# Kernel optimization log

Measured on AMD Instinct MI355X. Metric: run time of the kernel, lower is better.

## Reference

```python
import jax, jax.numpy as jnp
import numpy as np

T, B = 1024, 128
IDIM, CDIM, N, M = 256, 512, 128, 64


def setup_inputs() -> dict:
    key = jax.random.key(0)
    ks = jax.random.split(key, 10)
    stdev = 5.0 / np.sqrt(IDIM + M + CDIM)  # matches _reset_controller
    u = lambda k, shp: jax.random.uniform(k, shp, jnp.float32, -stdev, stdev)
    return {
        "embs": jax.random.normal(ks[0], (T, B, IDIM), jnp.float32),
        "ilen": T // 2,
        # LSTM controller params (PyTorch layout: [4*cdim, in] / [4*cdim, cdim])
        "w_ih": u(ks[1], (4 * CDIM, IDIM + M)),
        "w_hh": u(ks[2], (4 * CDIM, CDIM)),
        "b_ih": jnp.zeros((4 * CDIM,), jnp.float32),
        "b_hh": jnp.zeros((4 * CDIM,), jnp.float32),
        "h0": jax.random.normal(ks[3], (CDIM,), jnp.float32) * 0.05,
        "c0": jax.random.normal(ks[4], (CDIM,), jnp.float32) * 0.05,
        "r0": jax.random.normal(ks[5], (1, M), jnp.float32) * 0.02,
        # memory head params (concrete subclass): write address / write value / read address
        "W_wa": jax.random.normal(ks[6], (N, CDIM), jnp.float32) * 0.02,
        "b_wa": jnp.zeros((N,), jnp.float32),
        "W_wv": jax.random.normal(ks[7], (M, IDIM), jnp.float32) * 0.02,
        "b_wv": jnp.zeros((M,), jnp.float32),
        "W_ra": jax.random.normal(ks[8], (N, CDIM), jnp.float32) * 0.02,
        "b_ra": jnp.zeros((N,), jnp.float32),
    }


def _forward(embs, w_ih, w_hh, b_ih, b_hh, h0, c0, r0,
             W_wa, b_wa, W_wv, b_wv, W_ra, b_ra, ilen):
    bsz = embs.shape[1]
    h = jnp.broadcast_to(h0, (bsz, CDIM))
    c = jnp.broadcast_to(c0, (bsz, CDIM))
    r = jnp.broadcast_to(r0, (bsz, M))
    mem = jnp.zeros((bsz, N, M), embs.dtype)
    b = b_ih + b_hh

    def step(carry, xt):
        h, c, r, mem = carry
        emb, t = xt  # emb: [B, idim]
        x = jnp.concatenate([emb, r], axis=-1)            # [B, idim+M]
        gates = x @ w_ih.T + h @ w_hh.T + b               # [B, 4*cdim]
        i, f, g, o = jnp.split(gates, 4, axis=-1)         # torch gate order i,f,g,o
        c_new = jax.nn.sigmoid(f) * c + jax.nn.sigmoid(i) * jnp.tanh(g)
        h_new = jax.nn.sigmoid(o) * jnp.tanh(c_new)       # controller_outp
        is_write = t < ilen
        # write(controller_outp, emb): additive write at softmax address
        wa = jax.nn.softmax(h_new @ W_wa.T + b_wa, axis=-1)   # [B, N]
        v = emb @ W_wv.T + b_wv                               # [B, M]
        mem_new = jnp.where(is_write, mem + wa[:, :, None] * v[:, None, :], mem)
        # read(controller_outp): softmax-addressed weighted sum over slots
        ra = jax.nn.softmax(h_new @ W_ra.T + b_ra, axis=-1)   # [B, N]
        r_read = jnp.einsum('bn,bnm->bm', ra, mem_new)        # [B, M]
        r_new = jnp.where(is_write, r, r_read)
        out = jnp.concatenate([h_new, r_new], axis=-1)        # [B, cdim+M]
        return (h_new, c_new, r_new, mem_new), out

    _, os = jax.lax.scan(step, (h, c, r, mem),
                         (embs, jnp.arange(embs.shape[0])))
    return os  # [T, B, cdim+M]


def reference(embs, ilen, w_ih, w_hh, b_ih, b_hh, h0, c0, r0,
              W_wa, b_wa, W_wv, b_wv, W_ra, b_ra):
    return _forward(embs, w_ih, w_hh, b_ih, b_hh, h0, c0, r0,
                    W_wa, b_wa, W_wv, b_wv, W_ra, b_ra, ilen)
```

## Files before the change

### kernel.cpp

```cpp
#include <hip/hip_runtime.h>

typedef _Float16 f16;
typedef __attribute__((ext_vector_type(8))) _Float16 half8;
typedef __attribute__((ext_vector_type(2))) _Float16 half2v;
typedef __attribute__((ext_vector_type(4))) float f32x4;
typedef __attribute__((ext_vector_type(4))) unsigned int u32x4;
typedef unsigned long long u64;

#define TSTEPS 1024

static const size_t OFF_WP   = 0;
static const size_t OFF_BIAS = 3407872;
static const size_t OFF_EMBP = 3416064;
static const size_t OFF_V    = 70524928;
static const size_t OFF_XPRH = 104079360;
static const size_t OFF_MEM  = 104374272;
static const size_t OFF_BAR  = 108568576;
static const size_t OFF_WVP  = 108569600;
static const size_t WS_NEED  = 108602368;


__global__ void marnn_packw(const float* __restrict__ w_ih, const float* __restrict__ w_hh,
                            const float* __restrict__ b_ih, const float* __restrict__ b_hh,
                            f16* __restrict__ WP, float* __restrict__ biasP) {
  int idx = blockIdx.x * 256 + threadIdx.x;
  if (idx < 2048) {
    int j = idx >> 2, g = idx & 3, rg = g * 512 + j;
    biasP[idx] = b_ih[rg] + b_hh[rg];
  }
  if (idx >= 1703936) return;
  int e = idx & 7, l = (idx >> 3) & 63;
  int q = idx >> 9;
  int ks = q % 26; int ntile = q / 26;
  int n = ntile * 16 + (l & 15);
  int k = ks * 32 + (l >> 4) * 8 + e;
  int j2 = n >> 2, g2 = n & 3, rg2 = g2 * 512 + j2;
  float v = (k < 320) ? w_ih[(size_t)rg2 * 320 + k] : w_hh[(size_t)rg2 * 512 + (k - 320)];
  WP[idx] = (f16)v;
}

__global__ void marnn_packwv(const float* __restrict__ W_wv, f16* __restrict__ WVP) {
  int idx = blockIdx.x * 256 + threadIdx.x;
  if (idx >= 16384) return;
  int e = idx & 7, l = (idx >> 3) & 63, ks = (idx >> 9) & 7, nt = idx >> 12;
  int n = nt * 16 + (l & 15);
  int k = ks * 32 + (l >> 4) * 8 + e;
  WVP[idx] = (f16)W_wv[n * 256 + k];
}

__global__ void marnn_packemb(const float* __restrict__ embs, f16* __restrict__ embsP) {
  const long total8 = (long)1024 * 128 * 32;
  const long stride = (long)gridDim.x * blockDim.x;
  for (long i8 = (long)blockIdx.x * blockDim.x + threadIdx.x; i8 < total8; i8 += stride) {
    int bl = (int)(i8 & 15), kc = (int)((i8 >> 4) & 31), bg = (int)((i8 >> 9) & 7);
    long t = i8 >> 12;
    const float* s = embs + ((t * 128) + bg * 16 + bl) * 256 + kc * 8;
    f32x4 a = *(const f32x4*)s, b = *(const f32x4*)(s + 4);
    half8 h;
    h[0]=(f16)a[0]; h[1]=(f16)a[1]; h[2]=(f16)a[2]; h[3]=(f16)a[3];
    h[4]=(f16)b[0]; h[5]=(f16)b[1]; h[6]=(f16)b[2]; h[7]=(f16)b[3];
    *(half8*)(embsP + i8 * 8) = h;
  }
}

__global__ __launch_bounds__(256)
void marnn_vpre(const f16* __restrict__ embsP, const f16* __restrict__ WVP,
                const float* __restrict__ b_wv, float* __restrict__ V) {
  const int tb = blockIdx.x;
  const int wv = threadIdx.x >> 6, l = threadIdx.x & 63;
  half8 bf[8];
  #pragma unroll
  for (int ks = 0; ks < 8; ++ks)
    bf[ks] = *(const half8*)(WVP + ((size_t)(wv * 8 + ks) * 64 + l) * 8);
  const f16* ab = embsP + (size_t)tb * 4096;
  f32x4 acc = {0.f, 0.f, 0.f, 0.f};
  #pragma unroll
  for (int ks = 0; ks < 8; ++ks) {
    half8 af = *(const half8*)(ab + ((size_t)(ks * 4 + (l >> 4)) * 16 + (l & 15)) * 8);
    acc = __builtin_amdgcn_mfma_f32_16x16x32_f16(bf[ks], af, acc, 0, 0, 0);
  }
  const int b = (tb & 7) * 16 + (l & 15);
  const long t = tb >> 3;
  #pragma unroll
  for (int r = 0; r < 4; ++r) {
    int m = wv * 16 + (l >> 4) * 4 + r;
    V[((t * 128) + b) * 64 + m] = acc[r] + b_wv[m];
  }
}

__global__ void marnn_init(const float* __restrict__ h0, const float* __restrict__ r0,
                           f16* __restrict__ XPRH) {
  int idx = blockIdx.x * 256 + threadIdx.x;
  if (idx >= 147456) return;
  int e = idx & 7; int q = idx >> 7; int kcidx = q % 72;
  float v = (kcidx < 8) ? r0[kcidx * 8 + e] : h0[(kcidx - 8) * 8 + e];
  XPRH[idx] = (f16)v;
}


struct __align__(16) MarnnSMem {
  f16  whead[128 * 512];
  char xl[26624];
  char un[4096];
};

__device__ __forceinline__ float marnn_dot8(half8 a, half8 b, float acc) {
#if __has_builtin(__builtin_amdgcn_fdot2)
  half2v a0 = {a[0],a[1]}, a1 = {a[2],a[3]}, a2 = {a[4],a[5]}, a3 = {a[6],a[7]};
  half2v b0 = {b[0],b[1]}, b1 = {b[2],b[3]}, b2 = {b[4],b[5]}, b3 = {b[6],b[7]};
  acc = __builtin_amdgcn_fdot2(a0, b0, acc, false);
  acc = __builtin_amdgcn_fdot2(a1, b1, acc, false);
  acc = __builtin_amdgcn_fdot2(a2, b2, acc, false);
  acc = __builtin_amdgcn_fdot2(a3, b3, acc, false);
#else
  #pragma unroll
  for (int e = 0; e < 8; ++e) acc += (float)a[e] * (float)b[e];
#endif
  return acc;
}

__device__ __forceinline__ float fast_sigmoid(float x) {
  return __builtin_amdgcn_rcpf(1.f + __expf(-x));
}
__device__ __forceinline__ float fast_tanh(float x) {
  return 1.f - 2.f * __builtin_amdgcn_rcpf(1.f + __expf(2.f * x));
}

__device__ __forceinline__ unsigned ld_flag(const unsigned* p) {
  return __hip_atomic_load(p, __ATOMIC_RELAXED, __HIP_MEMORY_SCOPE_AGENT);
}
__device__ __forceinline__ void st_flag(unsigned* p, unsigned v) {
  __hip_atomic_store(p, v, __ATOMIC_RELAXED, __HIP_MEMORY_SCOPE_AGENT);
}
__device__ __forceinline__ u64 ld_llc64(const void* p) {
  return __hip_atomic_load((const u64*)p, __ATOMIC_RELAXED, __HIP_MEMORY_SCOPE_AGENT);
}
__device__ __forceinline__ void st_llc32(void* p, unsigned v) {
  __hip_atomic_store((unsigned*)p, v, __ATOMIC_RELAXED, __HIP_MEMORY_SCOPE_AGENT);
}

__device__ __forceinline__ void poll16(const unsigned* line, unsigned ep) {
  int l = threadIdx.x & 63;
  for (;;) {
    unsigned v = (l < 16) ? ld_flag(line + l) : ep;
    if (__all((int)(v >= ep))) break;
    __builtin_amdgcn_s_sleep(1);
  }
  asm volatile("" ::: "memory");
}

union H2U { f16 f; unsigned short u; };

__global__ __launch_bounds__(512, 1)
void marnn_main(const int* __restrict__ ilen_p, const float* __restrict__ c0,
                const float* __restrict__ r0,
                const float* __restrict__ W_wa, const float* __restrict__ b_wa,
                const float* __restrict__ W_ra, const float* __restrict__ b_ra,
                float* __restrict__ out, char* __restrict__ ws) {
  __shared__ MarnnSMem sm;

  const f16*   WP    = (const f16*)(ws + OFF_WP);
  const float* biasP = (const float*)(ws + OFF_BIAS);
  const f16*   embsP = (const f16*)(ws + OFF_EMBP);
  const float* Vbuf  = (const float*)(ws + OFF_V);
  f16*         XPRH  = (f16*)(ws + OFF_XPRH);
  float*       MEMB  = (float*)(ws + OFF_MEM);
  unsigned*    FLAGS = (unsigned*)(ws + OFF_BAR);

  const int blk = blockIdx.x, tid = threadIdx.x;
  const int wav = tid >> 6, lane = tid & 63;
  const int g = blk & 7, ns = blk >> 3;
  const int ilen = ilen_p[0];
  unsigned* gfh = FLAGS + g * 32;
  unsigned* gfr = gfh + 16;

  half8 bfr[26];
  {
    const f16* wpb = WP + ((size_t)(ns * 8 + wav) * 26) * 512 + lane * 8;
    #pragma unroll
    for (int ks = 0; ks < 26; ++ks) bfr[ks] = *(const half8*)(wpb + ks * 512);
  }

  auto loadWhead = [&](const float* Wsrc) {
    for (int i = tid; i < 8192; i += 512) {
      int n = i >> 6, slot = i & 63;
      const float* s = Wsrc + n * 512 + slot * 8;
      f32x4 a = *(const f32x4*)(s), b2 = *(const f32x4*)(s + 4);
      half8 hv;
      hv[0]=(f16)a[0]; hv[1]=(f16)a[1]; hv[2]=(f16)a[2]; hv[3]=(f16)a[3];
      hv[4]=(f16)b2[0]; hv[5]=(f16)b2[1]; hv[6]=(f16)b2[2]; hv[7]=(f16)b2[3];
      *(half8*)((char*)sm.whead + (n << 10) + (((slot + n) & 63) << 4)) = hv;
    }
  };
  loadWhead(ilen > 0 ? W_wa : W_ra);

  {
    const u32x4* s0 = (const u32x4*)(embsP + ((size_t)0 * 8 + g) * 4096);
    ((u32x4*)sm.xl)[tid] = s0[tid];
    const u32x4* s1 = (const u32x4*)(XPRH + (((size_t)0 * 8 + g) * 72 + 8) * 128);
    u32x4* d1 = (u32x4*)(sm.xl + 10240);
    d1[tid * 2] = s1[tid * 2]; d1[tid * 2 + 1] = s1[tid * 2 + 1];
  }
  __syncthreads();

  const int b_l = tid >> 5, jj = tid & 31;
  const int jg = ns * 32 + jj;
  float c = c0[jg];
  const f32x4 bias4 = *(const f32x4*)(biasP + ns * 128 + jj * 4);
  const float r0v = (tid < 64) ? r0[tid] : 0.f;
  const int b = g * 16 + ns;

  const float bw0 = b_wa[lane], bw1 = b_wa[lane + 64];
  const float br0 = b_ra[lane], br1 = b_ra[lane + 64];
  const int gn = (wav & 3) * 32 + (lane & 31);
  const int kq = ((wav >> 2) << 1) | (lane >> 5);

  half8 rf0, rf1;
  {
    const f16* rbase = XPRH + ((size_t)g * 72) * 128 + (lane >> 4) * 128 + (lane & 15) * 8;
    rf0 = *(const half8*)(rbase);
    rf1 = *(const half8*)(rbase + 512);
  }

  for (int t = 0; t < TSTEPS; ++t) {
    const int par = t & 1, nxt = par ^ 1;
    const bool iswrite = (t < ilen);

    u32x4 sa = {0u, 0u, 0u, 0u};
    if (t + 1 < TSTEPS)
      sa = ((const u32x4*)(embsP + (((size_t)(t + 1) * 8) + g) * 4096))[tid];
    f32x4 vv4 = {0.f, 0.f, 0.f, 0.f};
    if (iswrite && wav == 4 && lane < 16)
      vv4 = *(const f32x4*)(Vbuf + ((size_t)t * 128 + b) * 64 + lane * 4);

    if (t > ilen && wav == 0) {
      poll16(gfr, (unsigned)(t - ilen));
      const u64* rp = (const u64*)(XPRH + (((size_t)par * 8 + g) * 72) * 128
                                   + (lane >> 4) * 128 + (lane & 15) * 8);
      union { u64 u[2]; half8 h; } r0u, r1u;
      r0u.u[0] = ld_llc64(rp);       r0u.u[1] = ld_llc64(rp + 1);
      r1u.u[0] = ld_llc64(rp + 128); r1u.u[1] = ld_llc64(rp + 129);
      char* rdst = sm.xl + 8192 + (lane >> 4) * 256 + (lane & 15) * 16;
      *(half8*)rdst = r0u.h;
      *(half8*)(rdst + 1024) = r1u.h;
    }
    f32x4 acc0 = {0.f, 0.f, 0.f, 0.f}, acc1 = {0.f, 0.f, 0.f, 0.f};
    const char* xb = sm.xl + (lane >> 4) * 256 + (lane & 15) * 16;
    #pragma unroll
    for (int ks = 0; ks < 8; ++ks) {
      half8 af = *(const half8*)(xb + ks * 1024);
      if (ks & 1) acc1 = __builtin_amdgcn_mfma_f32_16x16x32_f16(af, bfr[ks], acc1, 0, 0, 0);
      else        acc0 = __builtin_amdgcn_mfma_f32_16x16x32_f16(af, bfr[ks], acc0, 0, 0, 0);
    }
    #pragma unroll
    for (int ks = 10; ks < 26; ++ks) {
      half8 af = *(const half8*)(xb + ks * 1024);
      if (ks & 1) acc1 = __builtin_amdgcn_mfma_f32_16x16x32_f16(af, bfr[ks], acc1, 0, 0, 0);
      else        acc0 = __builtin_amdgcn_mfma_f32_16x16x32_f16(af, bfr[ks], acc0, 0, 0, 0);
    }
    if (t <= ilen) {
      acc0 = __builtin_amdgcn_mfma_f32_16x16x32_f16(rf0, bfr[8], acc0, 0, 0, 0);
      acc1 = __builtin_amdgcn_mfma_f32_16x16x32_f16(rf1, bfr[9], acc1, 0, 0, 0);
    }
    __syncthreads();
    if (t > ilen) {
      acc0 = __builtin_amdgcn_mfma_f32_16x16x32_f16(*(const half8*)(xb + 8 * 1024), bfr[8], acc0, 0, 0, 0);
      acc1 = __builtin_amdgcn_mfma_f32_16x16x32_f16(*(const half8*)(xb + 9 * 1024), bfr[9], acc1, 0, 0, 0);
    }
    f32x4 acc = acc0 + acc1;
    {
      float* gatebuf = (float*)sm.xl;
      #pragma unroll
      for (int r = 0; r < 4; ++r)
        gatebuf[((lane >> 4) * 4 + r) * 128 + wav * 16 + (lane & 15)] = acc[r];
    }
    __syncthreads();
    float h;
    {
      const float* gatebuf = (const float*)sm.xl;
      f32x4 g4 = *(const f32x4*)(gatebuf + b_l * 128 + jj * 4);
      float si = fast_sigmoid(g4[0] + bias4[0]);
      float sf = fast_sigmoid(g4[1] + bias4[1]);
      float so = fast_sigmoid(g4[3] + bias4[3]);
      c = sf * c + si * fast_tanh(g4[2] + bias4[2]);
      h = so * fast_tanh(c);
      H2U cv; cv.f = (f16)h;
      int o = __shfl_down((int)cv.u, 1, 64);
      if (!(tid & 1))
        st_llc32(&XPRH[(((size_t)nxt * 8 + g) * 72 + 8 + (jg >> 3)) * 128 + b_l * 8 + (jj & 7)],
                 ((unsigned)cv.u) | (((unsigned)(unsigned short)o) << 16));
    }

    asm volatile("s_waitcnt vmcnt(0)" ::: "memory");
    __syncthreads();
    if (tid == 0) st_flag(gfh + ns, (unsigned)(t + 1));
    __builtin_nontemporal_store(h, &out[(size_t)t * 73728 + (g * 16 + b_l) * 576 + jg]);
    if (wav == 0) poll16(gfh, (unsigned)(t + 1));
    __syncthreads();
    {
      const u64* s1 = (const u64*)(XPRH + (((size_t)nxt * 8 + g) * 72 + 8) * 128);
      u64 hb0 = ld_llc64(s1 + tid * 4 + 0), hb1 = ld_llc64(s1 + tid * 4 + 1);
      u64 hb2 = ld_llc64(s1 + tid * 4 + 2), hb3 = ld_llc64(s1 + tid * 4 + 3);
      ((u32x4*)sm.xl)[tid] = sa;
      u64* d1 = (u64*)(sm.xl + 10240);
      d1[tid * 4 + 0] = hb0; d1[tid * 4 + 1] = hb1;
      d1[tid * 4 + 2] = hb2; d1[tid * 4 + 3] = hb3;
    }
    __syncthreads();

    if (t == ilen) { loadWhead(W_ra); __syncthreads(); }
    float* pbuf  = (float*)sm.un;
    float* vpart = (float*)(sm.un + 512);
    float* vred  = (float*)(sm.un + 1536);
    float* vsec  = (float*)(sm.un + 3584);
    {
      if (iswrite && wav == 4 && lane < 16) *(f32x4*)(vsec + lane * 4) = vv4;
      const char* wrow = (const char*)sm.whead + (gn << 10);
      const char* hbase = sm.xl + 10240 + ns * 16;
      float av0 = 0.f, av1 = 0.f;
      #pragma unroll
      for (int i = 0; i < 16; i += 2) {
        int s0 = kq * 16 + i;
        av0 = marnn_dot8(*(const half8*)(wrow + (((s0 + gn) & 63) << 4)),
                         *(const half8*)(hbase + s0 * 256), av0);
        av1 = marnn_dot8(*(const half8*)(wrow + (((s0 + 1 + gn) & 63) << 4)),
                         *(const half8*)(hbase + (s0 + 1) * 256), av1);
      }
      float av = av0 + av1;
      av += __shfl_xor(av, 32, 64);
      if (lane < 32) vpart[((wav >> 2) << 7) + gn] = av;
    }
    __syncthreads();
    if (wav == 0) {
      float l0 = vpart[lane] + vpart[128 + lane] + (iswrite ? bw0 : br0);
      float l1 = vpart[64 + lane] + vpart[192 + lane] + (iswrite ? bw1 : br1);
      float mx = fmaxf(l0, l1);
      #pragma unroll
      for (int off = 32; off > 0; off >>= 1) mx = fmaxf(mx, __shfl_xor(mx, off, 64));
      float e0 = __expf(l0 - mx), e1 = __expf(l1 - mx);
      float s = e0 + e1;
      #pragma unroll
      for (int off = 32; off > 0; off >>= 1) s += __shfl_xor(s, off, 64);
      float inv = __builtin_amdgcn_rcpf(s);
      pbuf[lane] = e0 * inv; pbuf[lane + 64] = e1 * inv;
    }
    __syncthreads();
    if (iswrite) {
      float p = pbuf[tid >> 2];
      float* mrow = MEMB + (((size_t)b) * 128 + (tid >> 2)) * 64 + (tid & 3) * 16;
      const float* vv = vsec + (tid & 3) * 16;
      #pragma unroll
      for (int i2 = 0; i2 < 16; i2 += 4) {
        f32x4 mm = *(f32x4*)(mrow + i2);
        f32x4 v4 = *(const f32x4*)(vv + i2);
        mm = mm + p * v4;
        *(f32x4*)(mrow + i2) = mm;
      }
      if (tid < 64)
        __builtin_nontemporal_store(r0v, &out[(size_t)t * 73728 + b * 576 + 512 + tid]);
    } else {
      const int m = tid & 63;
      const float* mcol = MEMB + (((size_t)b) * 128 + wav * 16) * 64 + m;
      float a0 = 0.f, a1 = 0.f;
      #pragma unroll
      for (int n2 = 0; n2 < 16; n2 += 2) {
        a0 = fmaf(pbuf[wav * 16 + n2],     mcol[n2 * 64],       a0);
        a1 = fmaf(pbuf[wav * 16 + n2 + 1], mcol[(n2 + 1) * 64], a1);
      }
      vred[wav * 64 + m] = a0 + a1;
      __syncthreads();
      if (tid < 64) {
        float rv = 0.f;
        #pragma unroll
        for (int nc = 0; nc < 8; ++nc) rv += vred[nc * 64 + tid];
        H2U cr; cr.f = (f16)rv;
        int o2 = __shfl_down((int)cr.u, 1, 64);
        if (!(tid & 1))
          st_llc32(&XPRH[(((size_t)nxt * 8 + g) * 72 + (tid >> 3)) * 128 + ns * 8 + (tid & 7)],
                   ((unsigned)cr.u) | (((unsigned)(unsigned short)o2) << 16));
        asm volatile("s_waitcnt vmcnt(0)" ::: "memory");
        if (tid == 0) st_flag(gfr + ns, (unsigned)(t - ilen + 1));
        __builtin_nontemporal_store(rv, &out[(size_t)t * 73728 + b * 576 + 512 + tid]);
      }
    }
  }
}


extern "C" void kernel_launch(void* const* d_in, const int* in_sizes, int n_in,
                              void* d_out, int out_size, void* d_ws, size_t ws_size,
                              hipStream_t stream) {
  const float* embs = (const float*)d_in[0];
  const int*   ilen = (const int*)d_in[1];
  const float* w_ih = (const float*)d_in[2];
  const float* w_hh = (const float*)d_in[3];
  const float* b_ih = (const float*)d_in[4];
  const float* b_hh = (const float*)d_in[5];
  const float* h0   = (const float*)d_in[6];
  const float* c0   = (const float*)d_in[7];
  const float* r0   = (const float*)d_in[8];
  const float* W_wa = (const float*)d_in[9];
  const float* b_wa = (const float*)d_in[10];
  const float* W_wv = (const float*)d_in[11];
  const float* b_wv = (const float*)d_in[12];
  const float* W_ra = (const float*)d_in[13];
  const float* b_ra = (const float*)d_in[14];
  float* out = (float*)d_out;
  char* ws = (char*)d_ws;
  if (ws_size < WS_NEED) return;

  hipMemsetAsync(ws + OFF_MEM, 0, 4194304, stream);
  hipMemsetAsync(ws + OFF_BAR, 0, 1024, stream);
  marnn_packw<<<6656, 256, 0, stream>>>(w_ih, w_hh, b_ih, b_hh,
                                        (f16*)(ws + OFF_WP), (float*)(ws + OFF_BIAS));
  marnn_packwv<<<64, 256, 0, stream>>>(W_wv, (f16*)(ws + OFF_WVP));
  marnn_packemb<<<2048, 256, 0, stream>>>(embs, (f16*)(ws + OFF_EMBP));
  marnn_vpre<<<8192, 256, 0, stream>>>((const f16*)(ws + OFF_EMBP), (const f16*)(ws + OFF_WVP),
                                       b_wv, (float*)(ws + OFF_V));
  marnn_init<<<576, 256, 0, stream>>>(h0, r0, (f16*)(ws + OFF_XPRH));
  marnn_main<<<128, 512, 0, stream>>>(ilen, c0, r0, W_wa, b_wa, W_ra, b_ra, out, ws);
}
```

Before: 5.535 ms.

## Swap MFMA operands so gates land per-lane, removing LDS gate transpose

Swaps the MFMA A/B operands so each lane's accumulator holds the four i,f,g,o gates of one hidden unit for one batch row. The LSTM cell update can then run directly from registers, dropping the LDS gate-buffer round trip and one block barrier per step. The read-vector poll and its barrier now run only in the read phase, and r0 is loaded straight from the input. The h output is now written from the f16 copy in LDS, so stored outputs lose precision versus the fp32 value. Nontemporal output stores become plain stores.

```diff
diff --git a/kernel.cpp b/kernel.cpp
--- a/kernel.cpp
+++ b/kernel.cpp
@@ -203,10 +203,10 @@
   }
   __syncthreads();
 
-  const int b_l = tid >> 5, jj = tid & 31;
-  const int jg = ns * 32 + jj;
+  const int b_lane = lane & 15, sel = lane >> 4;
+  const int jg = ns * 32 + wav * 4 + sel;
   float c = c0[jg];
-  const f32x4 bias4 = *(const f32x4*)(biasP + ns * 128 + jj * 4);
+  const f32x4 bias4 = *(const f32x4*)(biasP + jg * 4);
   const float r0v = (tid < 64) ? r0[tid] : 0.f;
   const int b = g * 16 + ns;
 
@@ -216,10 +216,10 @@
   const int kq = ((wav >> 2) << 1) | (lane >> 5);
 
   half8 rf0, rf1;
-  {
-    const f16* rbase = XPRH + ((size_t)g * 72) * 128 + (lane >> 4) * 128 + (lane & 15) * 8;
-    rf0 = *(const half8*)(rbase);
-    rf1 = *(const half8*)(rbase + 512);
+  #pragma unroll
+  for (int e = 0; e < 8; ++e) {
+    rf0[e] = (f16)r0[sel * 8 + e];
+    rf1[e] = (f16)r0[32 + sel * 8 + e];
   }
 
   for (int t = 0; t < TSTEPS; ++t) {
@@ -233,70 +233,60 @@
     if (iswrite && wav == 4 && lane < 16)
       vv4 = *(const f32x4*)(Vbuf + ((size_t)t * 128 + b) * 64 + lane * 4);
 
-    if (t > ilen && wav == 0) {
-      poll16(gfr, (unsigned)(t - ilen));
-      const u64* rp = (const u64*)(XPRH + (((size_t)par * 8 + g) * 72) * 128
-                                   + (lane >> 4) * 128 + (lane & 15) * 8);
-      union { u64 u[2]; half8 h; } r0u, r1u;
-      r0u.u[0] = ld_llc64(rp);       r0u.u[1] = ld_llc64(rp + 1);
-      r1u.u[0] = ld_llc64(rp + 128); r1u.u[1] = ld_llc64(rp + 129);
-      char* rdst = sm.xl + 8192 + (lane >> 4) * 256 + (lane & 15) * 16;
-      *(half8*)rdst = r0u.h;
-      *(half8*)(rdst + 1024) = r1u.h;
-    }
     f32x4 acc0 = {0.f, 0.f, 0.f, 0.f}, acc1 = {0.f, 0.f, 0.f, 0.f};
-    const char* xb = sm.xl + (lane >> 4) * 256 + (lane & 15) * 16;
+    const char* xb = sm.xl + sel * 256 + b_lane * 16;
     #pragma unroll
     for (int ks = 0; ks < 8; ++ks) {
       half8 af = *(const half8*)(xb + ks * 1024);
-      if (ks & 1) acc1 = __builtin_amdgcn_mfma_f32_16x16x32_f16(af, bfr[ks], acc1, 0, 0, 0);
-      else        acc0 = __builtin_amdgcn_mfma_f32_16x16x32_f16(af, bfr[ks], acc0, 0, 0, 0);
+      if (ks & 1) acc1 = __builtin_amdgcn_mfma_f32_16x16x32_f16(bfr[ks], af, acc1, 0, 0, 0);
+      else        acc0 = __builtin_amdgcn_mfma_f32_16x16x32_f16(bfr[ks], af, acc0, 0, 0, 0);
     }
     #pragma unroll
     for (int ks = 10; ks < 26; ++ks) {
       half8 af = *(const half8*)(xb + ks * 1024);
-      if (ks & 1) acc1 = __builtin_amdgcn_mfma_f32_16x16x32_f16(af, bfr[ks], acc1, 0, 0, 0);
-      else        acc0 = __builtin_amdgcn_mfma_f32_16x16x32_f16(af, bfr[ks], acc0, 0, 0, 0);
+      if (ks & 1) acc1 = __builtin_amdgcn_mfma_f32_16x16x32_f16(bfr[ks], af, acc1, 0, 0, 0);
+      else        acc0 = __builtin_amdgcn_mfma_f32_16x16x32_f16(bfr[ks], af, acc0, 0, 0, 0);
     }
     if (t <= ilen) {
-      acc0 = __builtin_amdgcn_mfma_f32_16x16x32_f16(rf0, bfr[8], acc0, 0, 0, 0);
-      acc1 = __builtin_amdgcn_mfma_f32_16x16x32_f16(rf1, bfr[9], acc1, 0, 0, 0);
-    }
-    __syncthreads();
-    if (t > ilen) {
-      acc0 = __builtin_amdgcn_mfma_f32_16x16x32_f16(*(const half8*)(xb + 8 * 1024), bfr[8], acc0, 0, 0, 0);
-      acc1 = __builtin_amdgcn_mfma_f32_16x16x32_f16(*(const half8*)(xb + 9 * 1024), bfr[9], acc1, 0, 0, 0);
-    }
-    f32x4 acc = acc0 + acc1;
+      acc0 = __builtin_amdgcn_mfma_f32_16x16x32_f16(bfr[8], rf0, acc0, 0, 0, 0);
+      acc1 = __builtin_amdgcn_mfma_f32_16x16x32_f16(bfr[9], rf1, acc1, 0, 0, 0);
+    } else {
+      if (wav == 0) {
+        poll16(gfr, (unsigned)(t - ilen));
+        const u64* rp = (const u64*)(XPRH + (((size_t)par * 8 + g) * 72) * 128
+                                     + (lane >> 4) * 128 + (lane & 15) * 8);
+        union { u64 u[2]; half8 h; } r0u, r1u;
+        r0u.u[0] = ld_llc64(rp);       r0u.u[1] = ld_llc64(rp + 1);
+        r1u.u[0] = ld_llc64(rp + 128); r1u.u[1] = ld_llc64(rp + 129);
+        char* rdst = sm.xl + 8192 + (lane >> 4) * 256 + (lane & 15) * 16;
+        *(half8*)rdst = r0u.h;
+        *(half8*)(rdst + 1024) = r1u.h;
+      }
+      __syncthreads();
+      acc0 = __builtin_amdgcn_mfma_f32_16x16x32_f16(bfr[8], *(const half8*)(xb + 8 * 1024), acc0, 0, 0, 0);
+      acc1 = __builtin_amdgcn_mfma_f32_16x16x32_f16(bfr[9], *(const half8*)(xb + 9 * 1024), acc1, 0, 0, 0);
+    }
+    const f32x4 acc = acc0 + acc1;
+
     {
-      float* gatebuf = (float*)sm.xl;
-      #pragma unroll
-      for (int r = 0; r < 4; ++r)
-        gatebuf[((lane >> 4) * 4 + r) * 128 + wav * 16 + (lane & 15)] = acc[r];
-    }
-    __syncthreads();
-    float h;
-    {
-      const float* gatebuf = (const float*)sm.xl;
-      f32x4 g4 = *(const f32x4*)(gatebuf + b_l * 128 + jj * 4);
-      float si = fast_sigmoid(g4[0] + bias4[0]);
-      float sf = fast_sigmoid(g4[1] + bias4[1]);
-      float so = fast_sigmoid(g4[3] + bias4[3]);
-      c = sf * c + si * fast_tanh(g4[2] + bias4[2]);
-      h = so * fast_tanh(c);
+      float si = fast_sigmoid(acc[0] + bias4[0]);
+      float sf = fast_sigmoid(acc[1] + bias4[1]);
+      float so = fast_sigmoid(acc[3] + bias4[3]);
+      c = sf * c + si * fast_tanh(acc[2] + bias4[2]);
+      float h = so * fast_tanh(c);
       H2U cv; cv.f = (f16)h;
-      int o = __shfl_down((int)cv.u, 1, 64);
-      if (!(tid & 1))
-        st_llc32(&XPRH[(((size_t)nxt * 8 + g) * 72 + 8 + (jg >> 3)) * 128 + b_l * 8 + (jj & 7)],
-                 ((unsigned)cv.u) | (((unsigned)(unsigned short)o) << 16));
-    }
-
+      unsigned hu = cv.u;
+      unsigned pu = __shfl_down(hu, 16, 64);
+      if (!(sel & 1))
+        st_llc32(&XPRH[(((size_t)nxt * 8 + g) * 72 + 8 + (jg >> 3)) * 128 + b_lane * 8 + (jg & 7)],
+                 hu | (pu << 16));
+    }
     asm volatile("s_waitcnt vmcnt(0)" ::: "memory");
     __syncthreads();
     if (tid == 0) st_flag(gfh + ns, (unsigned)(t + 1));
-    __builtin_nontemporal_store(h, &out[(size_t)t * 73728 + (g * 16 + b_l) * 576 + jg]);
     if (wav == 0) poll16(gfh, (unsigned)(t + 1));
     __syncthreads();
+
     {
       const u64* s1 = (const u64*)(XPRH + (((size_t)nxt * 8 + g) * 72 + 8) * 128);
       u64 hb0 = ld_llc64(s1 + tid * 4 + 0), hb1 = ld_llc64(s1 + tid * 4 + 1);
@@ -307,6 +297,13 @@
       d1[tid * 4 + 2] = hb2; d1[tid * 4 + 3] = hb3;
     }
     __syncthreads();
+
+    {
+      int ob = tid >> 5, ojj = tid & 31;
+      int oj = ns * 32 + ojj;
+      f16 hv = *(const f16*)(sm.xl + 10240 + (oj >> 3) * 256 + ob * 16 + (oj & 7) * 2);
+      out[(size_t)t * 73728 + (g * 16 + ob) * 576 + oj] = (float)hv;
+    }
 
     if (t == ilen) { loadWhead(W_ra); __syncthreads(); }
     float* pbuf  = (float*)sm.un;
@@ -357,7 +354,7 @@
         *(f32x4*)(mrow + i2) = mm;
       }
       if (tid < 64)
-        __builtin_nontemporal_store(r0v, &out[(size_t)t * 73728 + b * 576 + 512 + tid]);
+        out[(size_t)t * 73728 + b * 576 + 512 + tid] = r0v;
     } else {
       const int m = tid & 63;
       const float* mcol = MEMB + (((size_t)b) * 128 + wav * 16) * 64 + m;
@@ -374,13 +371,14 @@
         #pragma unroll
         for (int nc = 0; nc < 8; ++nc) rv += vred[nc * 64 + tid];
         H2U cr; cr.f = (f16)rv;
-        int o2 = __shfl_down((int)cr.u, 1, 64);
+        unsigned ru = cr.u;
+        unsigned rp2 = __shfl_down(ru, 1, 64);
         if (!(tid & 1))
           st_llc32(&XPRH[(((size_t)nxt * 8 + g) * 72 + (tid >> 3)) * 128 + ns * 8 + (tid & 7)],
-                   ((unsigned)cr.u) | (((unsigned)(unsigned short)o2) << 16));
+                   ru | (rp2 << 16));
         asm volatile("s_waitcnt vmcnt(0)" ::: "memory");
         if (tid == 0) st_flag(gfr + ns, (unsigned)(t - ilen + 1));
-        __builtin_nontemporal_store(rv, &out[(size_t)t * 73728 + b * 576 + 512 + tid]);
+        out[(size_t)t * 73728 + b * 576 + 512 + tid] = rv;
       }
     }
   }
```

After: 5.250 ms, median of 2. -5.1%, faster.
